# Kernel tuning notes

Hardware: AMD Instinct MI355X
Metric: run time of the kernel (lower is better)

The kernel has to match this reference:

```python
import jax, jax.numpy as jnp
import numpy as np

WIN_SIZE = 11
WIN_SIGMA = 1.5
DATA_RANGE = 255.0
K1, K2 = 0.01, 0.03


def _gauss_win():
    # matches _fspecial_gauss_1d(11, 1.5)
    coords = jnp.arange(WIN_SIZE, dtype=jnp.float32) - WIN_SIZE // 2
    g = jnp.exp(-(coords ** 2) / (2.0 * WIN_SIGMA ** 2))
    return g / g.sum()


def _gaussian_filter(x, win):
    # separable depthwise blur, 'valid' padding (padding=0 in torch), groups=C
    C = x.shape[1]
    dn = ('NCHW', 'OIHW', 'NCHW')
    kh = jnp.tile(win.reshape(1, 1, WIN_SIZE, 1), (C, 1, 1, 1))
    kw = jnp.tile(win.reshape(1, 1, 1, WIN_SIZE), (C, 1, 1, 1))
    out = jax.lax.conv_general_dilated(x, kh, (1, 1), 'VALID',
                                       dimension_numbers=dn, feature_group_count=C)
    out = jax.lax.conv_general_dilated(out, kw, (1, 1), 'VALID',
                                       dimension_numbers=dn, feature_group_count=C)
    return out


def setup_inputs() -> dict:
    key = jax.random.key(0)
    k1, k2 = jax.random.split(key)
    shape = (16, 3, 512, 512)
    X = jax.random.uniform(k1, shape, dtype=jnp.float32) * DATA_RANGE
    Y = jax.random.uniform(k2, shape, dtype=jnp.float32) * DATA_RANGE
    return {'X': X, 'Y': Y}


def reference(X, Y):
    win = _gauss_win()
    C1 = (K1 * DATA_RANGE) ** 2
    C2 = (K2 * DATA_RANGE) ** 2
    mu1 = _gaussian_filter(X, win)
    mu2 = _gaussian_filter(Y, win)
    mu1_sq = mu1 * mu1
    mu2_sq = mu2 * mu2
    mu1_mu2 = mu1 * mu2
    sigma1_sq = _gaussian_filter(X * X, win) - mu1_sq
    sigma2_sq = _gaussian_filter(Y * Y, win) - mu2_sq
    sigma12 = _gaussian_filter(X * Y, win) - mu1_mu2
    cs_map = (2.0 * sigma12 + C2) / (sigma1_sq + sigma2_sq + C2)
    ssim_map = (2.0 * mu1_mu2 + C1) / (mu1_sq + mu2_sq + C1) * cs_map
    # torch: mean over channel dim then squeeze(0) (no-op for N>1)
    ssim_map = jnp.mean(ssim_map, axis=1)  # [N, H-10, W-10]
    return 1.0 - ssim_map
```

## Files before the change

### kernel.cpp

```cpp
#include <hip/hip_runtime.h>


namespace {

constexpr int NN = 16, CC = 3, HH = 512, WW = 512;
constexpr int OH = HH - 10, OW = WW - 10;
constexpr int TW = 64, TH = 32;
constexpr int HPITCH = 56;
constexpr float C1c = 6.5025f;
constexpr float C2c = 58.5225f;

typedef _Float16 half8   __attribute__((ext_vector_type(8)));
typedef _Float16 half4   __attribute__((ext_vector_type(4)));
typedef float    floatv4 __attribute__((ext_vector_type(4)));

__device__ const float WF[11] = {
    0.00102838f, 0.00759876f, 0.03600077f, 0.10936069f, 0.21300553f,
    0.26601172f,
    0.21300553f, 0.10936069f, 0.03600077f, 0.00759876f, 0.00102838f
};

__device__ inline half8 pack8(const float4& a, const float4& b) {
    half8 h = {(_Float16)a.x, (_Float16)a.y, (_Float16)a.z, (_Float16)a.w,
               (_Float16)b.x, (_Float16)b.y, (_Float16)b.z, (_Float16)b.w};
    return h;
}

__global__ __launch_bounds__(256, 2)
void ssim_kernel(const float* __restrict__ X, const float* __restrict__ Y,
                 float* __restrict__ out)
{
    __shared__ __align__(16) _Float16 s_ht[2][TW][HPITCH];
    __shared__ _Float16 s_wtab[16];

    const int tid  = threadIdx.x;
    const int lane = tid & 63;
    const int wv   = tid >> 6;
    const int col0 = blockIdx.x * TW;
    const int row0 = blockIdx.y * TH;
    const int n    = blockIdx.z;

    if (tid < 16) s_wtab[tid] = (tid < 11) ? (_Float16)WF[tid] : (_Float16)0.f;
    __syncthreads();

    half8 bfrag;
    {
        const int bn = lane & 15, kq = (lane >> 4) * 8;
        #pragma unroll
        for (int j = 0; j < 8; ++j) {
            int kk = kq + j - bn;
            kk = (kk < 0 || kk > 10) ? 11 : kk;
            bfrag[j] = s_wtab[kk];
        }
    }

    const int arow = lane & 15;
    const int aq   = lane >> 4;
    const int crow = aq * 4;

    int gcol = col0 + wv * 16 + aq * 8;
    gcol = gcol <= WW - 8 ? gcol : WW - 8;
    int grow[3];
    #pragma unroll
    for (int rc = 0; rc < 3; ++rc) {
        int g = row0 + rc * 16 + arow;
        grow[rc] = g < HH ? g : HH - 1;
    }

    float acc[2][4] = {{0.f,0.f,0.f,0.f},{0.f,0.f,0.f,0.f}};

    const size_t plane = (size_t)HH * WW;
    const float* Xn = X + (size_t)n * CC * plane;
    const float* Yn = Y + (size_t)n * CC * plane;
    const floatv4 zf = {0.f, 0.f, 0.f, 0.f};

    float4 fx[3][2], fy[3][2];
    #pragma unroll
    for (int rc = 0; rc < 3; ++rc) {
        const float* bx = Xn + (size_t)grow[rc] * WW + gcol;
        const float* by = Yn + (size_t)grow[rc] * WW + gcol;
        fx[rc][0] = *(const float4*)bx;
        fx[rc][1] = *(const float4*)(bx + 4);
        fy[rc][0] = *(const float4*)by;
        fy[rc][1] = *(const float4*)(by + 4);
    }

    for (int ch = 0; ch < CC; ++ch) {
        half8 axf[3], ayf[3];
        #pragma unroll
        for (int rc = 0; rc < 3; ++rc) {
            axf[rc] = pack8(fx[rc][0], fx[rc][1]);
            ayf[rc] = pack8(fy[rc][0], fy[rc][1]);
        }

        if (ch + 1 < CC) {
            const float* Xc = Xn + (size_t)(ch + 1) * plane;
            const float* Yc = Yn + (size_t)(ch + 1) * plane;
            #pragma unroll
            for (int rc = 0; rc < 3; ++rc) {
                const float* bx = Xc + (size_t)grow[rc] * WW + gcol;
                const float* by = Yc + (size_t)grow[rc] * WW + gcol;
                fx[rc][0] = *(const float4*)bx;
                fx[rc][1] = *(const float4*)(bx + 4);
                fy[rc][0] = *(const float4*)by;
                fy[rc][1] = *(const float4*)(by + 4);
            }
        }

        floatv4 vfr[5][2];
        #pragma unroll
        for (int qi = 0; qi < 5; ++qi) {
            #pragma unroll
            for (int rc = 0; rc < 3; ++rc) {
                half8 a;
                if      (qi == 0) a = axf[rc] * ayf[rc];
                else if (qi == 1) a = axf[rc] * axf[rc];
                else if (qi == 2) a = axf[rc];
                else if (qi == 3) a = ayf[rc] * ayf[rc];
                else              a = ayf[rc];
                floatv4 d = __builtin_amdgcn_mfma_f32_16x16x32_f16(
                    a, bfrag, zf, 0, 0, 0);
                half4 h = {(_Float16)d[0], (_Float16)d[1],
                           (_Float16)d[2], (_Float16)d[3]};
                *(half4*)&s_ht[qi & 1][wv*16 + arow][rc*16 + crow] = h;
            }
            #pragma unroll
            for (int b = 0; b < 2; ++b) {
                half8 av = *(const half8*)
                    &s_ht[qi & 1][wv*16 + arow][b*16 + aq*8];
                vfr[qi][b] = __builtin_amdgcn_mfma_f32_16x16x32_f16(
                    av, bfrag, zf, 0, 0, 0);
            }
        }

        #pragma unroll
        for (int b = 0; b < 2; ++b) {
            #pragma unroll
            for (int p = 0; p < 4; ++p) {
                float m1 = vfr[2][b][p], m2 = vfr[4][b][p];
                float exx = vfr[1][b][p], eyy = vfr[3][b][p],
                      exy = vfr[0][b][p];
                float m1s = m1*m1, m2s = m2*m2, m12 = m1*m2;
                float s1 = exx - m1s, s2 = eyy - m2s, s12 = exy - m12;
                float n1 = 2.f*m12 + C1c, d1 = m1s + m2s + C1c;
                float n2 = 2.f*s12 + C2c, d2 = s1 + s2 + C2c;
                acc[b][p] = fmaf(n1 * n2, __builtin_amdgcn_rcpf(d1 * d2),
                                 acc[b][p]);
            }
        }
    }

    #pragma unroll
    for (int b = 0; b < 2; ++b) {
        const int orow = row0 + b*16 + arow;
        const int ocol = col0 + wv*16 + crow;
        if (orow < OH) {
            float r0v = 1.f - acc[b][0] * (1.f/3.f);
            float r1v = 1.f - acc[b][1] * (1.f/3.f);
            float r2v = 1.f - acc[b][2] * (1.f/3.f);
            float r3v = 1.f - acc[b][3] * (1.f/3.f);
            size_t base = ((size_t)n * OH + orow) * OW + ocol;
            if (ocol + 3 < OW) {
                *(float2*)(out + base)     = make_float2(r0v, r1v);
                *(float2*)(out + base + 2) = make_float2(r2v, r3v);
            } else {
                float rs[4] = {r0v, r1v, r2v, r3v};
                #pragma unroll
                for (int p = 0; p < 4; ++p)
                    if (ocol + p < OW) out[base + p] = rs[p];
            }
        }
    }
}

}

extern "C" void kernel_launch(void* const* d_in, const int* in_sizes, int n_in,
                              void* d_out, int out_size, void* d_ws, size_t ws_size,
                              hipStream_t stream) {
    const float* X = (const float*)d_in[0];
    const float* Y = (const float*)d_in[1];
    float* out = (float*)d_out;

    dim3 grid((OW + TW - 1) / TW,
              (OH + TH - 1) / TH,
              NN);
    ssim_kernel<<<grid, 256, 0, stream>>>(X, Y, out);
}
```

Before: 142.1 us.

## Process two row tiles per block with cross-tile prefetch and five LDS buffers

Each block now handles two vertical 32-row tiles in sequence, halving the grid height. The next channel's loads, or the next tile's first-channel loads, are prefetched while the current one computes. The five horizontal-pass results go into separate LDS buffers so all vertical MFMAs can be issued together. This amortises block setup and keeps loads in flight across tile boundaries, at the cost of more LDS per block, which may reduce occupancy, and fewer blocks for parallelism.

```diff
diff --git a/kernel.cpp b/kernel.cpp
--- a/kernel.cpp
+++ b/kernel.cpp
@@ -5,8 +5,8 @@
 
 constexpr int NN = 16, CC = 3, HH = 512, WW = 512;
 constexpr int OH = HH - 10, OW = WW - 10;
-constexpr int TW = 64, TH = 32;
-constexpr int HPITCH = 56;
+constexpr int TW = 64, TH = 32, RT = 2;
+constexpr int HP = 56;
 constexpr float C1c = 6.5025f;
 constexpr float C2c = 58.5225f;
 
@@ -30,14 +30,14 @@
 void ssim_kernel(const float* __restrict__ X, const float* __restrict__ Y,
                  float* __restrict__ out)
 {
-    __shared__ __align__(16) _Float16 s_ht[2][TW][HPITCH];
+    __shared__ __align__(16) _Float16 s_ht[5][TW][HP];
     __shared__ _Float16 s_wtab[16];
 
     const int tid  = threadIdx.x;
     const int lane = tid & 63;
     const int wv   = tid >> 6;
     const int col0 = blockIdx.x * TW;
-    const int row0 = blockIdx.y * TH;
+    const int rowB = blockIdx.y * (TH * RT);
     const int n    = blockIdx.z;
 
     if (tid < 16) s_wtab[tid] = (tid < 11) ? (_Float16)WF[tid] : (_Float16)0.f;
@@ -60,14 +60,16 @@
 
     int gcol = col0 + wv * 16 + aq * 8;
     gcol = gcol <= WW - 8 ? gcol : WW - 8;
-    int grow[3];
+    int voffs[RT][3];
     #pragma unroll
-    for (int rc = 0; rc < 3; ++rc) {
-        int g = row0 + rc * 16 + arow;
-        grow[rc] = g < HH ? g : HH - 1;
-    }
-
-    float acc[2][4] = {{0.f,0.f,0.f,0.f},{0.f,0.f,0.f,0.f}};
+    for (int t = 0; t < RT; ++t) {
+        #pragma unroll
+        for (int rc = 0; rc < 3; ++rc) {
+            int g = rowB + t * TH + rc * 16 + arow;
+            g = g < HH ? g : HH - 1;
+            voffs[t][rc] = g * WW + gcol;
+        }
+    }
 
     const size_t plane = (size_t)HH * WW;
     const float* Xn = X + (size_t)n * CC * plane;
@@ -77,98 +79,107 @@
     float4 fx[3][2], fy[3][2];
     #pragma unroll
     for (int rc = 0; rc < 3; ++rc) {
-        const float* bx = Xn + (size_t)grow[rc] * WW + gcol;
-        const float* by = Yn + (size_t)grow[rc] * WW + gcol;
+        const float* bx = Xn + voffs[0][rc];
+        const float* by = Yn + voffs[0][rc];
         fx[rc][0] = *(const float4*)bx;
         fx[rc][1] = *(const float4*)(bx + 4);
         fy[rc][0] = *(const float4*)by;
         fy[rc][1] = *(const float4*)(by + 4);
     }
 
-    for (int ch = 0; ch < CC; ++ch) {
-        half8 axf[3], ayf[3];
-        #pragma unroll
-        for (int rc = 0; rc < 3; ++rc) {
-            axf[rc] = pack8(fx[rc][0], fx[rc][1]);
-            ayf[rc] = pack8(fy[rc][0], fy[rc][1]);
-        }
-
-        if (ch + 1 < CC) {
-            const float* Xc = Xn + (size_t)(ch + 1) * plane;
-            const float* Yc = Yn + (size_t)(ch + 1) * plane;
+    float acc[2][4] = {{0.f,0.f,0.f,0.f},{0.f,0.f,0.f,0.f}};
+
+    #pragma unroll
+    for (int t = 0; t < RT; ++t) {
+        #pragma unroll
+        for (int ch = 0; ch < CC; ++ch) {
+            half8 axf[3], ayf[3];
             #pragma unroll
             for (int rc = 0; rc < 3; ++rc) {
-                const float* bx = Xc + (size_t)grow[rc] * WW + gcol;
-                const float* by = Yc + (size_t)grow[rc] * WW + gcol;
-                fx[rc][0] = *(const float4*)bx;
-                fx[rc][1] = *(const float4*)(bx + 4);
-                fy[rc][0] = *(const float4*)by;
-                fy[rc][1] = *(const float4*)(by + 4);
-            }
-        }
-
-        floatv4 vfr[5][2];
-        #pragma unroll
-        for (int qi = 0; qi < 5; ++qi) {
+                axf[rc] = pack8(fx[rc][0], fx[rc][1]);
+                ayf[rc] = pack8(fy[rc][0], fy[rc][1]);
+            }
+
+            const int nch = (ch == CC - 1) ? 0 : ch + 1;
+            const int nt  = (ch == CC - 1) ? t + 1 : t;
+            if (nt < RT) {
+                const float* Xc = Xn + (size_t)nch * plane;
+                const float* Yc = Yn + (size_t)nch * plane;
+                #pragma unroll
+                for (int rc = 0; rc < 3; ++rc) {
+                    const float* bx = Xc + voffs[nt][rc];
+                    const float* by = Yc + voffs[nt][rc];
+                    fx[rc][0] = *(const float4*)bx;
+                    fx[rc][1] = *(const float4*)(bx + 4);
+                    fy[rc][0] = *(const float4*)by;
+                    fy[rc][1] = *(const float4*)(by + 4);
+                }
+            }
+
             #pragma unroll
-            for (int rc = 0; rc < 3; ++rc) {
-                half8 a;
-                if      (qi == 0) a = axf[rc] * ayf[rc];
-                else if (qi == 1) a = axf[rc] * axf[rc];
-                else if (qi == 2) a = axf[rc];
-                else if (qi == 3) a = ayf[rc] * ayf[rc];
-                else              a = ayf[rc];
-                floatv4 d = __builtin_amdgcn_mfma_f32_16x16x32_f16(
-                    a, bfrag, zf, 0, 0, 0);
-                half4 h = {(_Float16)d[0], (_Float16)d[1],
-                           (_Float16)d[2], (_Float16)d[3]};
-                *(half4*)&s_ht[qi & 1][wv*16 + arow][rc*16 + crow] = h;
-            }
+            for (int qi = 0; qi < 5; ++qi) {
+                #pragma unroll
+                for (int rc = 0; rc < 3; ++rc) {
+                    half8 a;
+                    if      (qi == 0) a = axf[rc];
+                    else if (qi == 1) a = ayf[rc];
+                    else if (qi == 2) a = axf[rc] * axf[rc];
+                    else if (qi == 3) a = ayf[rc] * ayf[rc];
+                    else              a = axf[rc] * ayf[rc];
+                    floatv4 d = __builtin_amdgcn_mfma_f32_16x16x32_f16(
+                        a, bfrag, zf, 0, 0, 0);
+                    half4 h = {(_Float16)d[0], (_Float16)d[1],
+                               (_Float16)d[2], (_Float16)d[3]};
+                    *(half4*)&s_ht[qi][wv*16 + arow][rc*16 + crow] = h;
+                }
+            }
+
             #pragma unroll
             for (int b = 0; b < 2; ++b) {
-                half8 av = *(const half8*)
-                    &s_ht[qi & 1][wv*16 + arow][b*16 + aq*8];
-                vfr[qi][b] = __builtin_amdgcn_mfma_f32_16x16x32_f16(
-                    av, bfrag, zf, 0, 0, 0);
+                floatv4 v[5];
+                #pragma unroll
+                for (int qi = 0; qi < 5; ++qi) {
+                    half8 av = *(const half8*)
+                        &s_ht[qi][wv*16 + arow][b*16 + aq*8];
+                    v[qi] = __builtin_amdgcn_mfma_f32_16x16x32_f16(
+                        av, bfrag, zf, 0, 0, 0);
+                }
+                #pragma unroll
+                for (int p = 0; p < 4; ++p) {
+                    float m1 = v[0][p], m2 = v[1][p];
+                    float exx = v[2][p], eyy = v[3][p], exy = v[4][p];
+                    float m1s = m1*m1, m2s = m2*m2, m12 = m1*m2;
+                    float s1 = exx - m1s, s2 = eyy - m2s, s12 = exy - m12;
+                    float n1 = 2.f*m12 + C1c, d1 = m1s + m2s + C1c;
+                    float n2 = 2.f*s12 + C2c, d2 = s1 + s2 + C2c;
+                    acc[b][p] = fmaf(n1 * n2,
+                                     __builtin_amdgcn_rcpf(d1 * d2),
+                                     acc[b][p]);
+                }
             }
         }
 
         #pragma unroll
         for (int b = 0; b < 2; ++b) {
-            #pragma unroll
-            for (int p = 0; p < 4; ++p) {
-                float m1 = vfr[2][b][p], m2 = vfr[4][b][p];
-                float exx = vfr[1][b][p], eyy = vfr[3][b][p],
-                      exy = vfr[0][b][p];
-                float m1s = m1*m1, m2s = m2*m2, m12 = m1*m2;
-                float s1 = exx - m1s, s2 = eyy - m2s, s12 = exy - m12;
-                float n1 = 2.f*m12 + C1c, d1 = m1s + m2s + C1c;
-                float n2 = 2.f*s12 + C2c, d2 = s1 + s2 + C2c;
-                acc[b][p] = fmaf(n1 * n2, __builtin_amdgcn_rcpf(d1 * d2),
-                                 acc[b][p]);
-            }
-        }
-    }
-
-    #pragma unroll
-    for (int b = 0; b < 2; ++b) {
-        const int orow = row0 + b*16 + arow;
-        const int ocol = col0 + wv*16 + crow;
-        if (orow < OH) {
-            float r0v = 1.f - acc[b][0] * (1.f/3.f);
-            float r1v = 1.f - acc[b][1] * (1.f/3.f);
-            float r2v = 1.f - acc[b][2] * (1.f/3.f);
-            float r3v = 1.f - acc[b][3] * (1.f/3.f);
-            size_t base = ((size_t)n * OH + orow) * OW + ocol;
-            if (ocol + 3 < OW) {
-                *(float2*)(out + base)     = make_float2(r0v, r1v);
-                *(float2*)(out + base + 2) = make_float2(r2v, r3v);
-            } else {
-                float rs[4] = {r0v, r1v, r2v, r3v};
-                #pragma unroll
-                for (int p = 0; p < 4; ++p)
-                    if (ocol + p < OW) out[base + p] = rs[p];
-            }
+            const int orow = rowB + t * TH + b * 16 + arow;
+            const int ocol = col0 + wv * 16 + crow;
+            if (orow < OH) {
+                float r0v = 1.f - acc[b][0] * (1.f/3.f);
+                float r1v = 1.f - acc[b][1] * (1.f/3.f);
+                float r2v = 1.f - acc[b][2] * (1.f/3.f);
+                float r3v = 1.f - acc[b][3] * (1.f/3.f);
+                size_t base = ((size_t)n * OH + orow) * OW + ocol;
+                if (ocol + 3 < OW) {
+                    *(float2*)(out + base)     = make_float2(r0v, r1v);
+                    *(float2*)(out + base + 2) = make_float2(r2v, r3v);
+                } else {
+                    float rs[4] = {r0v, r1v, r2v, r3v};
+                    #pragma unroll
+                    for (int p = 0; p < 4; ++p)
+                        if (ocol + p < OW) out[base + p] = rs[p];
+                }
+            }
+            acc[b][0] = acc[b][1] = acc[b][2] = acc[b][3] = 0.f;
         }
     }
 }
@@ -183,7 +194,7 @@
     float* out = (float*)d_out;
 
     dim3 grid((OW + TW - 1) / TW,
-              (OH + TH - 1) / TH,
+              (OH + TH * RT - 1) / (TH * RT),
               NN);
     ssim_kernel<<<grid, 256, 0, stream>>>(X, Y, out);
 }
```

Result: slower. 148.0 us (+4.1%).

## Stage input tiles into LDS via async global_load_lds with double buffering

Applied to the files above, without the earlier changes.

Replaces the per-thread register prefetch of the X/Y input rows with direct global-to-LDS async loads (global_load_lds), double-buffered across channels. A manual waitcnt and barrier schedule lets the next channel's tile stream in while the current one is processed. Each tile is loaded once as a contiguous 48x80 block instead of overlapping per-wave fetches. In exchange it adds about 60KB of LDS, which may cap occupancy below the two blocks requested in launch bounds, plus extra barriers and an LDS read pass.

```diff
diff --git a/kernel.cpp b/kernel.cpp
--- a/kernel.cpp
+++ b/kernel.cpp
@@ -6,13 +6,23 @@
 constexpr int NN = 16, CC = 3, HH = 512, WW = 512;
 constexpr int OH = HH - 10, OW = WW - 10;
 constexpr int TW = 64, TH = 32;
+constexpr int SROWS = 48, SCOLS = 80;
+constexpr int SCH = SROWS * SCOLS;
 constexpr int HPITCH = 56;
 constexpr float C1c = 6.5025f;
 constexpr float C2c = 58.5225f;
 
+constexpr int WC_VM8 = 0xF78;
+constexpr int WC_VM6 = 0xF76;
+constexpr int WC_VM0 = 0xF70;
+constexpr int WC_LG0 = 0xC07F;
+
 typedef _Float16 half8   __attribute__((ext_vector_type(8)));
 typedef _Float16 half4   __attribute__((ext_vector_type(4)));
 typedef float    floatv4 __attribute__((ext_vector_type(4)));
+typedef unsigned int u32;
+typedef u32 __attribute__((address_space(1))) gu32;
+typedef u32 __attribute__((address_space(3))) lu32;
 
 __device__ const float WF[11] = {
     0.00102838f, 0.00759876f, 0.03600077f, 0.10936069f, 0.21300553f,
@@ -26,10 +36,15 @@
     return h;
 }
 
+__device__ inline void stage16(const float* g, void* l) {
+    __builtin_amdgcn_global_load_lds((const gu32*)g, (lu32*)l, 16, 0, 0);
+}
+
 __global__ __launch_bounds__(256, 2)
 void ssim_kernel(const float* __restrict__ X, const float* __restrict__ Y,
                  float* __restrict__ out)
 {
+    __shared__ __align__(16) float s_in[2][2][SCH];
     __shared__ __align__(16) _Float16 s_ht[2][TW][HPITCH];
     __shared__ _Float16 s_wtab[16];
 
@@ -58,54 +73,73 @@
     const int aq   = lane >> 4;
     const int crow = aq * 4;
 
-    int gcol = col0 + wv * 16 + aq * 8;
-    gcol = gcol <= WW - 8 ? gcol : WW - 8;
-    int grow[3];
+    int sOff[4];
+    const int sCnt = (wv < 3) ? 4 : 3;
     #pragma unroll
-    for (int rc = 0; rc < 3; ++rc) {
-        int g = row0 + rc * 16 + arow;
-        grow[rc] = g < HH ? g : HH - 1;
-    }
-
-    float acc[2][4] = {{0.f,0.f,0.f,0.f},{0.f,0.f,0.f,0.f}};
+    for (int i = 0; i < 4; ++i) {
+        const int c  = (wv * 4 + i) * 64 + lane;
+        const int r  = c / 20;
+        const int c4 = c - r * 20;
+        int gr = row0 + r;        gr = gr < HH ? gr : HH - 1;
+        int gc = col0 + c4 * 4;   gc = gc <= WW - 4 ? gc : WW - 4;
+        sOff[i] = gr * WW + gc;
+    }
 
     const size_t plane = (size_t)HH * WW;
     const float* Xn = X + (size_t)n * CC * plane;
     const float* Yn = Y + (size_t)n * CC * plane;
+
+    auto STAGE = [&](int nc, int b) {
+        const float* Xc = Xn + (size_t)nc * plane;
+        const float* Yc = Yn + (size_t)nc * plane;
+        #pragma unroll
+        for (int i = 0; i < 4; ++i) {
+            if (i < sCnt) {
+                char* lx = (char*)&s_in[b][0][0] + (wv * 4 + i) * 1024;
+                char* ly = (char*)&s_in[b][1][0] + (wv * 4 + i) * 1024;
+                stage16(Xc + sOff[i], lx);
+                stage16(Yc + sOff[i], ly);
+            }
+        }
+    };
+
+    STAGE(0, 0);
+    STAGE(1, 1);
+
+    float acc[2][4] = {{0.f,0.f,0.f,0.f},{0.f,0.f,0.f,0.f}};
     const floatv4 zf = {0.f, 0.f, 0.f, 0.f};
-
-    float4 fx[3][2], fy[3][2];
-    #pragma unroll
-    for (int rc = 0; rc < 3; ++rc) {
-        const float* bx = Xn + (size_t)grow[rc] * WW + gcol;
-        const float* by = Yn + (size_t)grow[rc] * WW + gcol;
-        fx[rc][0] = *(const float4*)bx;
-        fx[rc][1] = *(const float4*)(bx + 4);
-        fy[rc][0] = *(const float4*)by;
-        fy[rc][1] = *(const float4*)(by + 4);
-    }
+    const int cbase = wv * 16 + aq * 8;
 
     for (int ch = 0; ch < CC; ++ch) {
+        const int b = ch & 1;
+
+        if (ch < 2) {
+            if (wv < 3) __builtin_amdgcn_s_waitcnt(WC_VM8);
+            else        __builtin_amdgcn_s_waitcnt(WC_VM6);
+        } else {
+            __builtin_amdgcn_s_waitcnt(WC_VM0);
+        }
+        __builtin_amdgcn_sched_barrier(0);
+        __builtin_amdgcn_s_barrier();
+        __builtin_amdgcn_sched_barrier(0);
+
         half8 axf[3], ayf[3];
         #pragma unroll
         for (int rc = 0; rc < 3; ++rc) {
-            axf[rc] = pack8(fx[rc][0], fx[rc][1]);
-            ayf[rc] = pack8(fy[rc][0], fy[rc][1]);
-        }
-
-        if (ch + 1 < CC) {
-            const float* Xc = Xn + (size_t)(ch + 1) * plane;
-            const float* Yc = Yn + (size_t)(ch + 1) * plane;
-            #pragma unroll
-            for (int rc = 0; rc < 3; ++rc) {
-                const float* bx = Xc + (size_t)grow[rc] * WW + gcol;
-                const float* by = Yc + (size_t)grow[rc] * WW + gcol;
-                fx[rc][0] = *(const float4*)bx;
-                fx[rc][1] = *(const float4*)(bx + 4);
-                fy[rc][0] = *(const float4*)by;
-                fy[rc][1] = *(const float4*)(by + 4);
-            }
-        }
+            const int idx = (rc * 16 + arow) * SCOLS + cbase;
+            float4 a0 = *(const float4*)&s_in[b][0][idx];
+            float4 a1 = *(const float4*)&s_in[b][0][idx + 4];
+            float4 b0 = *(const float4*)&s_in[b][1][idx];
+            float4 b1 = *(const float4*)&s_in[b][1][idx + 4];
+            axf[rc] = pack8(a0, a1);
+            ayf[rc] = pack8(b0, b1);
+        }
+        __builtin_amdgcn_s_waitcnt(WC_LG0);
+        __builtin_amdgcn_sched_barrier(0);
+        __builtin_amdgcn_s_barrier();
+        __builtin_amdgcn_sched_barrier(0);
+
+        if (ch == 0) STAGE(2, 0);
 
         floatv4 vfr[5][2];
         #pragma unroll
@@ -125,40 +159,40 @@
                 *(half4*)&s_ht[qi & 1][wv*16 + arow][rc*16 + crow] = h;
             }
             #pragma unroll
-            for (int b = 0; b < 2; ++b) {
+            for (int bb = 0; bb < 2; ++bb) {
                 half8 av = *(const half8*)
-                    &s_ht[qi & 1][wv*16 + arow][b*16 + aq*8];
-                vfr[qi][b] = __builtin_amdgcn_mfma_f32_16x16x32_f16(
+                    &s_ht[qi & 1][wv*16 + arow][bb*16 + aq*8];
+                vfr[qi][bb] = __builtin_amdgcn_mfma_f32_16x16x32_f16(
                     av, bfrag, zf, 0, 0, 0);
             }
         }
 
         #pragma unroll
-        for (int b = 0; b < 2; ++b) {
+        for (int bb = 0; bb < 2; ++bb) {
             #pragma unroll
             for (int p = 0; p < 4; ++p) {
-                float m1 = vfr[2][b][p], m2 = vfr[4][b][p];
-                float exx = vfr[1][b][p], eyy = vfr[3][b][p],
-                      exy = vfr[0][b][p];
+                float m1 = vfr[2][bb][p], m2 = vfr[4][bb][p];
+                float exx = vfr[1][bb][p], eyy = vfr[3][bb][p],
+                      exy = vfr[0][bb][p];
                 float m1s = m1*m1, m2s = m2*m2, m12 = m1*m2;
                 float s1 = exx - m1s, s2 = eyy - m2s, s12 = exy - m12;
                 float n1 = 2.f*m12 + C1c, d1 = m1s + m2s + C1c;
                 float n2 = 2.f*s12 + C2c, d2 = s1 + s2 + C2c;
-                acc[b][p] = fmaf(n1 * n2, __builtin_amdgcn_rcpf(d1 * d2),
-                                 acc[b][p]);
+                acc[bb][p] = fmaf(n1 * n2, __builtin_amdgcn_rcpf(d1 * d2),
+                                  acc[bb][p]);
             }
         }
     }
 
     #pragma unroll
-    for (int b = 0; b < 2; ++b) {
-        const int orow = row0 + b*16 + arow;
+    for (int bb = 0; bb < 2; ++bb) {
+        const int orow = row0 + bb*16 + arow;
         const int ocol = col0 + wv*16 + crow;
         if (orow < OH) {
-            float r0v = 1.f - acc[b][0] * (1.f/3.f);
-            float r1v = 1.f - acc[b][1] * (1.f/3.f);
-            float r2v = 1.f - acc[b][2] * (1.f/3.f);
-            float r3v = 1.f - acc[b][3] * (1.f/3.f);
+            float r0v = 1.f - acc[bb][0] * (1.f/3.f);
+            float r1v = 1.f - acc[bb][1] * (1.f/3.f);
+            float r2v = 1.f - acc[bb][2] * (1.f/3.f);
+            float r3v = 1.f - acc[bb][3] * (1.f/3.f);
             size_t base = ((size_t)n * OH + orow) * OW + ocol;
             if (ocol + 3 < OW) {
                 *(float2*)(out + base)     = make_float2(r0v, r1v);
```

Result: faster. 134.0 us (-5.7%).

## Stage all channels' input tiles into LDS as fp16 with coalesced loads

Applied to the files above, without the earlier changes.

Replaces the per-thread strided 8-float row loads with a cooperative, coalesced load of the whole 48x80 input halo for all three channels of X and Y. The tiles are converted to fp16 and stored in shared memory, and MFMA A-fragments are then read from there. All global loads are issued up front to increase memory-level parallelism. The intermediate buffer loses its double-buffering and the occupancy hint rises from 2 to 3 blocks per CU. This adds a large LDS footprint (about 46KB) and many live registers for the prefetch. The single-buffered intermediate buffer also reuses the same LDS slot across qi iterations with no explicit barrier, relying on each wave touching only its own rows.

```diff
diff --git a/kernel.cpp b/kernel.cpp
--- a/kernel.cpp
+++ b/kernel.cpp
@@ -6,6 +6,8 @@
 constexpr int NN = 16, CC = 3, HH = 512, WW = 512;
 constexpr int OH = HH - 10, OW = WW - 10;
 constexpr int TW = 64, TH = 32;
+constexpr int SR = 48, SC = 80;
+constexpr int PIT = 80;
 constexpr int HPITCH = 56;
 constexpr float C1c = 6.5025f;
 constexpr float C2c = 58.5225f;
@@ -20,17 +22,12 @@
     0.21300553f, 0.10936069f, 0.03600077f, 0.00759876f, 0.00102838f
 };
 
-__device__ inline half8 pack8(const float4& a, const float4& b) {
-    half8 h = {(_Float16)a.x, (_Float16)a.y, (_Float16)a.z, (_Float16)a.w,
-               (_Float16)b.x, (_Float16)b.y, (_Float16)b.z, (_Float16)b.w};
-    return h;
-}
-
-__global__ __launch_bounds__(256, 2)
+__global__ __launch_bounds__(256, 3)
 void ssim_kernel(const float* __restrict__ X, const float* __restrict__ Y,
                  float* __restrict__ out)
 {
-    __shared__ __align__(16) _Float16 s_ht[2][TW][HPITCH];
+    __shared__ __align__(16) _Float16 s_f16[CC][2][SR * PIT];
+    __shared__ __align__(16) _Float16 s_ht[TW][HPITCH];
     __shared__ _Float16 s_wtab[16];
 
     const int tid  = threadIdx.x;
@@ -58,53 +55,63 @@
     const int aq   = lane >> 4;
     const int crow = aq * 4;
 
-    int gcol = col0 + wv * 16 + aq * 8;
-    gcol = gcol <= WW - 8 ? gcol : WW - 8;
-    int grow[3];
+    const int sCnt = (wv < 3) ? 4 : 3;
+    int srcOff[4], ldsOff[4];
     #pragma unroll
-    for (int rc = 0; rc < 3; ++rc) {
-        int g = row0 + rc * 16 + arow;
-        grow[rc] = g < HH ? g : HH - 1;
+    for (int i = 0; i < 4; ++i) {
+        const int c  = (wv * 4 + i) * 64 + lane;
+        const int r  = c / 20;
+        const int c4 = c - r * 20;
+        int gr = row0 + r;        gr = gr < HH ? gr : HH - 1;
+        int gc = col0 + c4 * 4;   gc = gc <= WW - 4 ? gc : WW - 4;
+        srcOff[i] = gr * WW + gc;
+        ldsOff[i] = r * PIT + c4 * 4;
     }
-
-    float acc[2][4] = {{0.f,0.f,0.f,0.f},{0.f,0.f,0.f,0.f}};
 
     const size_t plane = (size_t)HH * WW;
     const float* Xn = X + (size_t)n * CC * plane;
     const float* Yn = Y + (size_t)n * CC * plane;
+
+    float4 L[CC][2][4];
+    #pragma unroll
+    for (int ch = 0; ch < CC; ++ch) {
+        #pragma unroll
+        for (int i = 0; i < 4; ++i) {
+            if (i < sCnt) {
+                L[ch][0][i] = *(const float4*)(Xn + (size_t)ch * plane + srcOff[i]);
+                L[ch][1][i] = *(const float4*)(Yn + (size_t)ch * plane + srcOff[i]);
+            }
+        }
+    }
+
+    #pragma unroll
+    for (int ch = 0; ch < CC; ++ch) {
+        #pragma unroll
+        for (int s = 0; s < 2; ++s) {
+            #pragma unroll
+            for (int i = 0; i < 4; ++i) {
+                if (i < sCnt) {
+                    float4 v = L[ch][s][i];
+                    half4 h = {(_Float16)v.x, (_Float16)v.y,
+                               (_Float16)v.z, (_Float16)v.w};
+                    *(half4*)&s_f16[ch][s][ldsOff[i]] = h;
+                }
+            }
+        }
+    }
+    __syncthreads();
+
+    float acc[2][4] = {{0.f,0.f,0.f,0.f},{0.f,0.f,0.f,0.f}};
     const floatv4 zf = {0.f, 0.f, 0.f, 0.f};
-
-    float4 fx[3][2], fy[3][2];
-    #pragma unroll
-    for (int rc = 0; rc < 3; ++rc) {
-        const float* bx = Xn + (size_t)grow[rc] * WW + gcol;
-        const float* by = Yn + (size_t)grow[rc] * WW + gcol;
-        fx[rc][0] = *(const float4*)bx;
-        fx[rc][1] = *(const float4*)(bx + 4);
-        fy[rc][0] = *(const float4*)by;
-        fy[rc][1] = *(const float4*)(by + 4);
-    }
+    const int cbase = wv * 16 + aq * 8;
 
     for (int ch = 0; ch < CC; ++ch) {
         half8 axf[3], ayf[3];
         #pragma unroll
         for (int rc = 0; rc < 3; ++rc) {
-            axf[rc] = pack8(fx[rc][0], fx[rc][1]);
-            ayf[rc] = pack8(fy[rc][0], fy[rc][1]);
-        }
-
-        if (ch + 1 < CC) {
-            const float* Xc = Xn + (size_t)(ch + 1) * plane;
-            const float* Yc = Yn + (size_t)(ch + 1) * plane;
-            #pragma unroll
-            for (int rc = 0; rc < 3; ++rc) {
-                const float* bx = Xc + (size_t)grow[rc] * WW + gcol;
-                const float* by = Yc + (size_t)grow[rc] * WW + gcol;
-                fx[rc][0] = *(const float4*)bx;
-                fx[rc][1] = *(const float4*)(bx + 4);
-                fy[rc][0] = *(const float4*)by;
-                fy[rc][1] = *(const float4*)(by + 4);
-            }
+            const int idx = (rc * 16 + arow) * PIT + cbase;
+            axf[rc] = *(const half8*)&s_f16[ch][0][idx];
+            ayf[rc] = *(const half8*)&s_f16[ch][1][idx];
         }
 
         floatv4 vfr[5][2];
@@ -122,12 +129,11 @@
                     a, bfrag, zf, 0, 0, 0);
                 half4 h = {(_Float16)d[0], (_Float16)d[1],
                            (_Float16)d[2], (_Float16)d[3]};
-                *(half4*)&s_ht[qi & 1][wv*16 + arow][rc*16 + crow] = h;
+                *(half4*)&s_ht[wv*16 + arow][rc*16 + crow] = h;
             }
             #pragma unroll
             for (int b = 0; b < 2; ++b) {
-                half8 av = *(const half8*)
-                    &s_ht[qi & 1][wv*16 + arow][b*16 + aq*8];
+                half8 av = *(const half8*)&s_ht[wv*16 + arow][b*16 + aq*8];
                 vfr[qi][b] = __builtin_amdgcn_mfma_f32_16x16x32_f16(
                     av, bfrag, zf, 0, 0, 0);
             }
```

Result: faster. 135.9 us (-4.4%).
